# Performance work log

Hardware: AMD Instinct MI355X
Metric: run time of the kernel (lower is better)

Reference implementation:

```python
import math
import jax, jax.numpy as jnp
import numpy as np

N_NODES = 200000          # len(tree)
HIDDEN = 1024             # args.hidden_dim
SINGLE_DIM = HIDDEN // 2  # lower/upper halves of the circle embedding
TREE_HEIGHT = 8           # path length (root-to-leaf)
BATCH = 2048              # positive pairs per step
N_NEG = 8                 # args.negative_sample_size
CIRCLE_MARGIN = 1.0       # args.circle_margin
SCR = 2.0 * math.pi       # single_circle_range


def setup_inputs() -> dict:
    key = jax.random.key(0)
    k1, k2, k3 = jax.random.split(key, 3)
    node_embedding = jax.random.normal(k1, (N_NODES, HIDDEN), dtype=jnp.float32)
    pos_path = jax.random.randint(k2, (BATCH, 2, TREE_HEIGHT), 0, N_NODES, dtype=jnp.int32)
    neg_path = jax.random.randint(k3, (BATCH, N_NEG, TREE_HEIGHT), 0, N_NODES, dtype=jnp.int32)
    return {"node_embedding": node_embedding, "pos_path": pos_path, "neg_path": neg_path}


def _inter_size(p1, p2):
    # |set(path1) & set(path2)| assuming distinct ids within a path.
    # p1: [..., P], p2: [..., P] -> [...]
    return (p1[..., :, None] == p2[..., None, :]).any(-1).sum(-1)


def _calc_dist(emb, p1, p2, diff):
    # emb: [V, H]; p1, p2: [..., P] int; diff: [...] float
    d = emb[p1] - emb[p2]                       # [..., P, H]
    low, high = d[..., :SINGLE_DIM], d[..., SINGLE_DIM:]
    dist = (0.5 * (low + high)).sum(-2)         # [..., SINGLE_DIM]
    return dist + (diff - 1.0)[..., None] * SCR


def reference(node_embedding, pos_path, neg_path):
    p1 = pos_path[:, 0]                          # [B, P]
    p2 = pos_path[:, 1]                          # [B, P]
    # calc_dist clamps diff to >= 1; calc_diff (used for k) does NOT.
    diff_pos = jnp.maximum(TREE_HEIGHT - _inter_size(p1, p2), 1).astype(jnp.float32)
    pos_dist = _calc_dist(node_embedding, p1, p2, diff_pos)          # [B, SD]

    diff_neg_raw = (TREE_HEIGHT - _inter_size(p1[:, None, :], neg_path)).astype(jnp.float32)  # [B, N]
    k = diff_neg_raw - 1.0                                            # unclamped, per source
    diff_neg = jnp.maximum(diff_neg_raw, 1.0)
    neg_dist = _calc_dist(node_embedding, p1[:, None, :], neg_path, diff_neg)  # [B, N, SD]

    tmp = k[..., None] * CIRCLE_MARGIN * SCR + pos_dist[:, None, :] - neg_dist  # [B, N, SD]
    tmp_p = jnp.maximum(tmp, 0.0)
    punish = jnp.sqrt((tmp_p * tmp_p).sum(-1)).sum()   # sum of per-(b,n) L2 norms
    return punish.reshape(1)
```

## Files before the change

### kernel.cpp

```cpp
#include <hip/hip_runtime.h>

constexpr int   TH    = 8;
constexpr int   NNEG  = 8;
constexpr int   HID4  = 256;
constexpr int   HALF4 = 128;
constexpr float SCR_F = 6.2831853071795864769f;

__global__ void zero_kernel(float* out) { out[0] = 0.0f; }

__global__ __launch_bounds__(128)
void punish_kernel(const float* __restrict__ emb,
                   const int*   __restrict__ pos_path,
                   const int*   __restrict__ neg_path,
                   float*       __restrict__ out)
{
    const int b = blockIdx.x;
    const int t = threadIdx.x;

    __shared__ int   s_p1[TH];
    __shared__ int   s_p2[TH];
    __shared__ int   s_neg[NNEG * TH];
    __shared__ float s_C[NNEG];
    __shared__ float s_red[2][NNEG];

    if (t < TH) {
        s_p1[t] = pos_path[b * 2 * TH + t];
        s_p2[t] = pos_path[b * 2 * TH + TH + t];
    }
    if (t < NNEG * TH) {
        s_neg[t] = neg_path[b * NNEG * TH + t];
    }
    __syncthreads();

    if (t < NNEG) {
        int inter_pos = 0;
#pragma unroll
        for (int i = 0; i < TH; i++) {
            const int v = s_p1[i];
            bool f = false;
#pragma unroll
            for (int j = 0; j < TH; j++) f = f || (v == s_p2[j]);
            inter_pos += f ? 1 : 0;
        }
        const float diff_pos = fmaxf((float)(TH - inter_pos), 1.0f);

        const int n = t;
        int inter_n = 0;
#pragma unroll
        for (int i = 0; i < TH; i++) {
            const int v = s_p1[i];
            bool f = false;
#pragma unroll
            for (int j = 0; j < TH; j++) f = f || (v == s_neg[n * TH + j]);
            inter_n += f ? 1 : 0;
        }
        const int raw = TH - inter_n;
        s_C[n] = (diff_pos - 1.0f - (raw == 0 ? 1.0f : 0.0f)) * SCR_F;
    }
    __syncthreads();

    const float4* __restrict__ embv = (const float4*)emb;

    float4 sp2 = {0.f, 0.f, 0.f, 0.f};
#pragma unroll
    for (int h = 0; h < TH; h++) {
        const float4* row = embv + (long)s_p2[h] * HID4;
        const float4 lo = row[t];
        const float4 hi = row[HALF4 + t];
        sp2.x += lo.x + hi.x;
        sp2.y += lo.y + hi.y;
        sp2.z += lo.z + hi.z;
        sp2.w += lo.w + hi.w;
    }

    float a[NNEG];
#pragma unroll
    for (int n = 0; n < NNEG; n++) {
        float4 sn = {0.f, 0.f, 0.f, 0.f};
#pragma unroll
        for (int h = 0; h < TH; h++) {
            const float4* row = embv + (long)s_neg[n * TH + h] * HID4;
            const float4 lo = row[t];
            const float4 hi = row[HALF4 + t];
            sn.x += lo.x + hi.x;
            sn.y += lo.y + hi.y;
            sn.z += lo.z + hi.z;
            sn.w += lo.w + hi.w;
        }
        const float c = s_C[n];
        float vx = c + 0.5f * (sn.x - sp2.x);
        float vy = c + 0.5f * (sn.y - sp2.y);
        float vz = c + 0.5f * (sn.z - sp2.z);
        float vw = c + 0.5f * (sn.w - sp2.w);
        vx = fmaxf(vx, 0.f); vy = fmaxf(vy, 0.f);
        vz = fmaxf(vz, 0.f); vw = fmaxf(vw, 0.f);
        a[n] = vx * vx + vy * vy + vz * vz + vw * vw;
    }

#pragma unroll
    for (int n = 0; n < NNEG; n++) {
#pragma unroll
        for (int off = 32; off > 0; off >>= 1) {
            a[n] += __shfl_down(a[n], off, 64);
        }
    }
    const int lane = t & 63;
    const int wid  = t >> 6;
    if (lane == 0) {
#pragma unroll
        for (int n = 0; n < NNEG; n++) s_red[wid][n] = a[n];
    }
    __syncthreads();

    if (t == 0) {
        float total = 0.f;
#pragma unroll
        for (int n = 0; n < NNEG; n++) {
            total += sqrtf(s_red[0][n] + s_red[1][n]);
        }
        atomicAdd(out, total);
    }
}

extern "C" void kernel_launch(void* const* d_in, const int* in_sizes, int n_in,
                              void* d_out, int out_size, void* d_ws, size_t ws_size,
                              hipStream_t stream) {
    const float* emb      = (const float*)d_in[0];
    const int*   pos_path = (const int*)d_in[1];
    const int*   neg_path = (const int*)d_in[2];
    float*       out      = (float*)d_out;

    const int BATCH = in_sizes[1] / (2 * TH);

    zero_kernel<<<1, 1, 0, stream>>>(out);
    punish_kernel<<<BATCH, 128, 0, stream>>>(emb, pos_path, neg_path, out);
}
```

Baseline: 966.0 us.

## Read path indices via scalar loads, drop LDS staging, replace atomic with two-stage reduction

New measurement: 990.4 us. +2.5%, slower.

```diff
diff --git a/kernel.cpp b/kernel.cpp
--- a/kernel.cpp
+++ b/kernel.cpp
@@ -2,71 +2,45 @@
 
 constexpr int   TH    = 8;
 constexpr int   NNEG  = 8;
-constexpr int   HID4  = 256;
-constexpr int   HALF4 = 128;
+constexpr int   HID   = 1024;
+constexpr int   HALF  = 512;
 constexpr float SCR_F = 6.2831853071795864769f;
-
-__global__ void zero_kernel(float* out) { out[0] = 0.0f; }
 
 __global__ __launch_bounds__(128)
 void punish_kernel(const float* __restrict__ emb,
                    const int*   __restrict__ pos_path,
                    const int*   __restrict__ neg_path,
-                   float*       __restrict__ out)
+                   float*       __restrict__ partial)
 {
     const int b = blockIdx.x;
     const int t = threadIdx.x;
 
-    __shared__ int   s_p1[TH];
-    __shared__ int   s_p2[TH];
-    __shared__ int   s_neg[NNEG * TH];
-    __shared__ float s_C[NNEG];
-    __shared__ float s_red[2][NNEG];
+    const int* __restrict__ pp = pos_path + b * (2 * TH);
+    const int* __restrict__ np = neg_path + b * (NNEG * TH);
 
-    if (t < TH) {
-        s_p1[t] = pos_path[b * 2 * TH + t];
-        s_p2[t] = pos_path[b * 2 * TH + TH + t];
+    int p1[TH], p2[TH];
+#pragma unroll
+    for (int h = 0; h < TH; h++) {
+        p1[h] = __builtin_amdgcn_readfirstlane(pp[h]);
+        p2[h] = __builtin_amdgcn_readfirstlane(pp[TH + h]);
     }
-    if (t < NNEG * TH) {
-        s_neg[t] = neg_path[b * NNEG * TH + t];
+
+    int inter_pos = 0;
+#pragma unroll
+    for (int i = 0; i < TH; i++) {
+        bool f = false;
+#pragma unroll
+        for (int j = 0; j < TH; j++) f = f || (p1[i] == p2[j]);
+        inter_pos += f ? 1 : 0;
     }
-    __syncthreads();
-
-    if (t < NNEG) {
-        int inter_pos = 0;
-#pragma unroll
-        for (int i = 0; i < TH; i++) {
-            const int v = s_p1[i];
-            bool f = false;
-#pragma unroll
-            for (int j = 0; j < TH; j++) f = f || (v == s_p2[j]);
-            inter_pos += f ? 1 : 0;
-        }
-        const float diff_pos = fmaxf((float)(TH - inter_pos), 1.0f);
-
-        const int n = t;
-        int inter_n = 0;
-#pragma unroll
-        for (int i = 0; i < TH; i++) {
-            const int v = s_p1[i];
-            bool f = false;
-#pragma unroll
-            for (int j = 0; j < TH; j++) f = f || (v == s_neg[n * TH + j]);
-            inter_n += f ? 1 : 0;
-        }
-        const int raw = TH - inter_n;
-        s_C[n] = (diff_pos - 1.0f - (raw == 0 ? 1.0f : 0.0f)) * SCR_F;
-    }
-    __syncthreads();
-
-    const float4* __restrict__ embv = (const float4*)emb;
+    const float diff_pos = fmaxf((float)(TH - inter_pos), 1.0f);
 
     float4 sp2 = {0.f, 0.f, 0.f, 0.f};
 #pragma unroll
     for (int h = 0; h < TH; h++) {
-        const float4* row = embv + (long)s_p2[h] * HID4;
-        const float4 lo = row[t];
-        const float4 hi = row[HALF4 + t];
+        const float* row = emb + (size_t)(unsigned)p2[h] * HID;
+        const float4 lo = *(const float4*)(row + 4 * t);
+        const float4 hi = *(const float4*)(row + HALF + 4 * t);
         sp2.x += lo.x + hi.x;
         sp2.y += lo.y + hi.y;
         sp2.z += lo.z + hi.z;
@@ -76,24 +50,37 @@
     float a[NNEG];
 #pragma unroll
     for (int n = 0; n < NNEG; n++) {
+        int ng[TH];
+#pragma unroll
+        for (int h = 0; h < TH; h++)
+            ng[h] = __builtin_amdgcn_readfirstlane(np[n * TH + h]);
+
+        int inter_n = 0;
+#pragma unroll
+        for (int i = 0; i < TH; i++) {
+            bool f = false;
+#pragma unroll
+            for (int j = 0; j < TH; j++) f = f || (p1[i] == ng[j]);
+            inter_n += f ? 1 : 0;
+        }
+        const int raw = TH - inter_n;
+        const float c = (diff_pos - 1.0f - (raw == 0 ? 1.0f : 0.0f)) * SCR_F;
+
         float4 sn = {0.f, 0.f, 0.f, 0.f};
 #pragma unroll
         for (int h = 0; h < TH; h++) {
-            const float4* row = embv + (long)s_neg[n * TH + h] * HID4;
-            const float4 lo = row[t];
-            const float4 hi = row[HALF4 + t];
+            const float* row = emb + (size_t)(unsigned)ng[h] * HID;
+            const float4 lo = *(const float4*)(row + 4 * t);
+            const float4 hi = *(const float4*)(row + HALF + 4 * t);
             sn.x += lo.x + hi.x;
             sn.y += lo.y + hi.y;
             sn.z += lo.z + hi.z;
             sn.w += lo.w + hi.w;
         }
-        const float c = s_C[n];
-        float vx = c + 0.5f * (sn.x - sp2.x);
-        float vy = c + 0.5f * (sn.y - sp2.y);
-        float vz = c + 0.5f * (sn.z - sp2.z);
-        float vw = c + 0.5f * (sn.w - sp2.w);
-        vx = fmaxf(vx, 0.f); vy = fmaxf(vy, 0.f);
-        vz = fmaxf(vz, 0.f); vw = fmaxf(vw, 0.f);
+        float vx = fmaxf(c + 0.5f * (sn.x - sp2.x), 0.f);
+        float vy = fmaxf(c + 0.5f * (sn.y - sp2.y), 0.f);
+        float vz = fmaxf(c + 0.5f * (sn.z - sp2.z), 0.f);
+        float vw = fmaxf(c + 0.5f * (sn.w - sp2.w), 0.f);
         a[n] = vx * vx + vy * vy + vz * vz + vw * vw;
     }
 
@@ -104,6 +91,8 @@
             a[n] += __shfl_down(a[n], off, 64);
         }
     }
+
+    __shared__ float s_red[2][NNEG];
     const int lane = t & 63;
     const int wid  = t >> 6;
     if (lane == 0) {
@@ -115,11 +104,27 @@
     if (t == 0) {
         float total = 0.f;
 #pragma unroll
-        for (int n = 0; n < NNEG; n++) {
+        for (int n = 0; n < NNEG; n++)
             total += sqrtf(s_red[0][n] + s_red[1][n]);
-        }
-        atomicAdd(out, total);
+        partial[b] = total;
     }
+}
+
+__global__ __launch_bounds__(256)
+void reduce_kernel(const float* __restrict__ partial, float* __restrict__ out,
+                   int n)
+{
+    const int t = threadIdx.x;
+    float s = 0.f;
+    for (int i = t; i < n; i += 256) s += partial[i];
+#pragma unroll
+    for (int off = 32; off > 0; off >>= 1) s += __shfl_down(s, off, 64);
+
+    __shared__ float s_w[4];
+    const int lane = t & 63, wid = t >> 6;
+    if (lane == 0) s_w[wid] = s;
+    __syncthreads();
+    if (t == 0) out[0] = s_w[0] + s_w[1] + s_w[2] + s_w[3];
 }
 
 extern "C" void kernel_launch(void* const* d_in, const int* in_sizes, int n_in,
@@ -129,9 +134,10 @@
     const int*   pos_path = (const int*)d_in[1];
     const int*   neg_path = (const int*)d_in[2];
     float*       out      = (float*)d_out;
+    float*       partial  = (float*)d_ws;
 
     const int BATCH = in_sizes[1] / (2 * TH);
 
-    zero_kernel<<<1, 1, 0, stream>>>(out);
-    punish_kernel<<<BATCH, 128, 0, stream>>>(emb, pos_path, neg_path, out);
+    punish_kernel<<<BATCH, 128, 0, stream>>>(emb, pos_path, neg_path, partial);
+    reduce_kernel<<<1, 256, 0, stream>>>(partial, out, BATCH);
 }
```
